# Kernel tuning notes

Measured on AMD Instinct MI355X. Metric: run time of the kernel, lower is better.

## Reference

```python
import jax, jax.numpy as jnp
import numpy as np

N = 100000      # nodes
E = 1600000     # directed edges (avg degree 16)
F_IN = 128
HID = 128
C = 40
EPS = 1e-5      # BatchNorm1d default eps


def setup_inputs() -> dict:
    key = jax.random.key(0)
    ks = jax.random.split(key, 8)
    f32 = jnp.float32
    x = jax.random.normal(ks[0], (N, F_IN), f32)
    edge_index = jax.random.randint(ks[1], (2, E), 0, N, dtype=jnp.int32)
    # Glorot-ish init for GCNConv linear weights
    W1 = jax.random.normal(ks[2], (F_IN, HID), f32) / np.float32(np.sqrt(F_IN))
    W2 = jax.random.normal(ks[3], (HID, HID), f32) / np.float32(np.sqrt(HID))
    W3 = jax.random.normal(ks[4], (HID, C), f32) / np.float32(np.sqrt(HID))
    return {
        "x": x, "edge_index": edge_index,
        "W1": W1, "b1": jnp.zeros((HID,), f32),
        "gamma1": jnp.ones((HID,), f32), "beta1": jnp.zeros((HID,), f32),
        "W2": W2, "b2": jnp.zeros((HID,), f32),
        "gamma2": jnp.ones((HID,), f32), "beta2": jnp.zeros((HID,), f32),
        "W3": W3, "b3": jnp.zeros((C,), f32),
    }


def _gcn_norm(edge_index):
    # PyG GCNConv default: add self loops, symmetric normalization
    loops = jnp.arange(N, dtype=edge_index.dtype)
    row = jnp.concatenate([edge_index[0], loops])  # source
    col = jnp.concatenate([edge_index[1], loops])  # destination
    deg = jax.ops.segment_sum(jnp.ones(row.shape[0], jnp.float32), col, num_segments=N)
    dinv = jnp.where(deg > 0, jax.lax.rsqrt(deg), 0.0)
    norm = dinv[row] * dinv[col]  # [E+N]
    return row, col, norm


def _gcn_conv(h, W, b, row, col, norm):
    h = h @ W                                   # [N, out]
    msg = h[row] * norm[:, None]                # gather + scale per edge
    out = jax.ops.segment_sum(msg, col, num_segments=N)
    return out + b


def _batchnorm(h, gamma, beta):
    # training-mode batch statistics (biased variance), as torch BatchNorm1d
    mean = h.mean(axis=0)
    var = ((h - mean) ** 2).mean(axis=0)
    return gamma * (h - mean) * jax.lax.rsqrt(var + EPS) + beta


def reference(x, edge_index, W1, b1, gamma1, beta1, W2, b2, gamma2, beta2, W3, b3):
    row, col, norm = _gcn_norm(edge_index)
    h = _gcn_conv(x, W1, b1, row, col, norm)
    h = jax.nn.relu(_batchnorm(h, gamma1, beta1))
    h = _gcn_conv(h, W2, b2, row, col, norm)
    h = jax.nn.relu(_batchnorm(h, gamma2, beta2))
    h = _gcn_conv(h, W3, b3, row, col, norm)
    return jax.nn.log_softmax(h, axis=1)
```

## Files before the change

kernel.cpp:

```cpp
#include <hip/hip_runtime.h>
#include <math.h>

#define N_NODES 100000
#define N_EDGES 1600000
#define NCLS 40
#define BN_EPS 1e-5f

#define BSPAN 256
#define NBKT 391
#define GBIN 256
#define CHUNK (N_EDGES / GBIN)
#define ECAP 5120

typedef unsigned int u32;
typedef unsigned short u16;
typedef __attribute__((ext_vector_type(8))) short bf16x8;
typedef __attribute__((ext_vector_type(4))) float f32x4;

__device__ inline float bl_lo(u32 u) { u32 x = u << 16; return __builtin_bit_cast(float, x); }
__device__ inline float bl_hi(u32 u) { u32 x = u & 0xFFFF0000u; return __builtin_bit_cast(float, x); }
__device__ inline u16 f2bl(float f) {
    u32 x = __builtin_bit_cast(u32, f);
    return (u16)((x + 0x7FFFu + ((x >> 16) & 1u)) >> 16);
}
__device__ inline u32 pk2(float lo, float hi) { return (u32)f2bl(lo) | ((u32)f2bl(hi) << 16); }

__global__ __launch_bounds__(256) void binA_kernel(const int* __restrict__ ei,
                                                   u32* __restrict__ ebuf,
                                                   int* __restrict__ runstart) {
    __shared__ int hist[NBKT];
    __shared__ int tmp[256];
    const int s = blockIdx.x, tid = threadIdx.x;
    const int e0 = s * CHUNK;

    for (int b = tid; b < NBKT; b += 256) hist[b] = 0;
    __syncthreads();
    for (int j = tid; j < CHUNK; j += 256) {
        int dst = ei[N_EDGES + e0 + j];
        atomicAdd(&hist[dst >> 8], 1);
    }
    __syncthreads();
    int i0 = 2 * tid, i1 = 2 * tid + 1;
    int a = (i0 < NBKT) ? hist[i0] : 0;
    int c = (i1 < NBKT) ? hist[i1] : 0;
    int ps = a + c;
    tmp[tid] = ps;
    __syncthreads();
    for (int o = 1; o < 256; o <<= 1) {
        int t = (tid >= o) ? tmp[tid - o] : 0;
        __syncthreads();
        tmp[tid] += t;
        __syncthreads();
    }
    int excl = tmp[tid] - ps;
    if (i0 < NBKT) hist[i0] = excl;
    if (i1 < NBKT) hist[i1] = excl + a;
    __syncthreads();
    for (int b = tid; b < NBKT; b += 256) runstart[b * GBIN + s] = hist[b];
    if (tid == 0) runstart[NBKT * GBIN + s] = CHUNK;
    __syncthreads();
    for (int j = tid; j < CHUNK; j += 256) {
        int src = ei[e0 + j];
        int dst = ei[N_EDGES + e0 + j];
        int p = atomicAdd(&hist[dst >> 8], 1);
        ebuf[e0 + p] = (u32)src | ((u32)(dst & 255) << 17);
    }
}

__global__ __launch_bounds__(256) void binC_kernel(const u32* __restrict__ ebuf,
                                                   const int* __restrict__ runstart,
                                                   int* __restrict__ csr, int* __restrict__ offs,
                                                   float* __restrict__ dinv) {
    __shared__ int srcs[ECAP];
    __shared__ unsigned char dl8[ECAP];
    __shared__ int sorted[ECAP + BSPAN];
    __shared__ int nodecnt[BSPAN];
    __shared__ int cursor[BSPAN];
    __shared__ int tmp[256];
    __shared__ int sbase;
    const int b = blockIdx.x, tid = threadIdx.x;
    const int nb0 = b * BSPAN;
    const int nnod = min(BSPAN, N_NODES - nb0);

    int r0 = runstart[b * GBIN + tid];
    int r1 = runstart[(b + 1) * GBIN + tid];
    int len = r1 - r0;

    tmp[tid] = r0;
    __syncthreads();
    for (int o = 128; o >= 1; o >>= 1) {
        if (tid < o) tmp[tid] += tmp[tid + o];
        __syncthreads();
    }
    if (tid == 0) sbase = tmp[0] + nb0;
    __syncthreads();
    const int base = sbase;

    tmp[tid] = len;
    __syncthreads();
    for (int o = 1; o < 256; o <<= 1) {
        int t = (tid >= o) ? tmp[tid - o] : 0;
        __syncthreads();
        tmp[tid] += t;
        __syncthreads();
    }
    int myoff = tmp[tid] - len;
    int total_e = tmp[255];
    if (total_e > ECAP) total_e = ECAP;
    for (int n = tid; n < BSPAN; n += 256) nodecnt[n] = 0;
    __syncthreads();
    const u32* seg = ebuf + (size_t)tid * CHUNK + r0;
    for (int j = 0; j < len; ++j) {
        int idx = myoff + j;
        if (idx >= ECAP) break;
        u32 p = seg[j];
        srcs[idx] = (int)(p & 0x1FFFFu);
        int dl = (int)(p >> 17);
        dl8[idx] = (unsigned char)dl;
        atomicAdd(&nodecnt[dl], 1);
    }
    __syncthreads();
    int cnt = (tid < nnod) ? (nodecnt[tid] + 1) : 0;
    tmp[tid] = cnt;
    __syncthreads();
    for (int o = 1; o < 256; o <<= 1) {
        int t = (tid >= o) ? tmp[tid - o] : 0;
        __syncthreads();
        tmp[tid] += t;
        __syncthreads();
    }
    int noff = tmp[tid] - cnt;
    if (tid < nnod) {
        cursor[tid] = noff + 1;
        sorted[noff] = nb0 + tid;
        offs[nb0 + tid] = base + noff;
        dinv[nb0 + tid] = rsqrtf((float)(nodecnt[tid] + 1));
    }
    if (b == NBKT - 1 && tid == 0) offs[N_NODES] = N_EDGES + N_NODES;
    __syncthreads();
    for (int idx = tid; idx < total_e; idx += 256) {
        int dl = dl8[idx];
        int p = atomicAdd(&cursor[dl], 1);
        sorted[p] = srcs[idx];
    }
    __syncthreads();
    int tot = total_e + nnod;
    for (int idx = tid; idx < tot; idx += 256) csr[base + idx] = sorted[idx];
}

__global__ void prep_w(const float* __restrict__ W1, const float* __restrict__ W2,
                       const float* __restrict__ W3, u16* __restrict__ Wt1,
                       u16* __restrict__ Wt2, u16* __restrict__ Wt3) {
    int b = blockIdx.x, t = threadIdx.x;
    if (b == 0) {
        for (int idx = t; idx < 128 * 128; idx += 256) {
            int c = idx >> 7, k = idx & 127;
            Wt1[idx] = f2bl(W1[k * 128 + c]);
        }
    } else if (b == 1) {
        for (int idx = t; idx < 128 * 128; idx += 256) {
            int c = idx >> 7, k = idx & 127;
            Wt2[idx] = f2bl(W2[k * 128 + c]);
        }
    } else {
        for (int idx = t; idx < 48 * 128; idx += 256) {
            int c = idx >> 7, k = idx & 127;
            Wt3[idx] = (c < NCLS) ? f2bl(W3[k * NCLS + c]) : (u16)0;
        }
    }
}

template <bool FOLD, bool IN_BF16, int BN, int OUTMODE>
__global__ __launch_bounds__(256) void mfma_gemm(const void* __restrict__ Xv,
                                                 const u16* __restrict__ Wt,
                                                 const float* __restrict__ ac,
                                                 const float* __restrict__ dinv,
                                                 void* __restrict__ Yv) {
    __shared__ __align__(16) u16 sX[64 * 128];
    __shared__ __align__(16) u16 sW[BN * 128];
    const int tid = threadIdx.x;
    const int row0 = blockIdx.x * 64;

    for (int ci = tid; ci < BN * 16; ci += 256) {
        int n = ci >> 4, ch = ci & 15;
        uint4 v = *(const uint4*)(Wt + n * 128 + ch * 8);
        *(uint4*)&sW[n * 128 + ((ch ^ (n & 7)) * 8)] = v;
    }
    {
        int r = tid >> 2;
        int gr = row0 + r;
        if (gr >= N_NODES) gr = N_NODES - 1;
        #pragma unroll
        for (int i = 0; i < 4; ++i) {
            int ch = (tid & 3) * 4 + i;
            int k0 = ch * 8;
            float xv[8];
            if (IN_BF16) {
                uint4 v = *((const uint4*)Xv + (size_t)gr * 16 + ch);
                xv[0] = bl_lo(v.x); xv[1] = bl_hi(v.x);
                xv[2] = bl_lo(v.y); xv[3] = bl_hi(v.y);
                xv[4] = bl_lo(v.z); xv[5] = bl_hi(v.z);
                xv[6] = bl_lo(v.w); xv[7] = bl_hi(v.w);
            } else {
                float4 p = *((const float4*)Xv + (size_t)gr * 32 + ch * 2);
                float4 q = *((const float4*)Xv + (size_t)gr * 32 + ch * 2 + 1);
                xv[0] = p.x; xv[1] = p.y; xv[2] = p.z; xv[3] = p.w;
                xv[4] = q.x; xv[5] = q.y; xv[6] = q.z; xv[7] = q.w;
            }
            if (FOLD) {
                #pragma unroll
                for (int j = 0; j < 8; ++j)
                    xv[j] = fmaxf(fmaf(xv[j], ac[k0 + j], ac[128 + k0 + j]), 0.f);
            }
            uint4 w;
            w.x = pk2(xv[0], xv[1]); w.y = pk2(xv[2], xv[3]);
            w.z = pk2(xv[4], xv[5]); w.w = pk2(xv[6], xv[7]);
            *(uint4*)&sX[r * 128 + ((ch ^ (r & 7)) * 8)] = w;
        }
    }
    __syncthreads();

    const int w = tid >> 6, l = tid & 63;
    const int g = l >> 4;
    const int lrow = w * 16 + (l & 15);
    bf16x8 afrag[4];
    #pragma unroll
    for (int kc = 0; kc < 4; ++kc) {
        int ch = kc * 4 + g;
        afrag[kc] = *(const bf16x8*)&sX[lrow * 128 + ((ch ^ (lrow & 7)) * 8)];
    }
    float sc[4];
    #pragma unroll
    for (int r = 0; r < 4; ++r) {
        int row = row0 + w * 16 + g * 4 + r;
        sc[r] = (row < N_NODES) ? dinv[row] : 0.f;
    }
    #pragma unroll
    for (int cg = 0; cg < BN / 16; ++cg) {
        const int n = cg * 16 + (l & 15);
        f32x4 acc = {0.f, 0.f, 0.f, 0.f};
        #pragma unroll
        for (int kc = 0; kc < 4; ++kc) {
            int ch = kc * 4 + g;
            bf16x8 bfrag = *(const bf16x8*)&sW[n * 128 + ((ch ^ (n & 7)) * 8)];
            acc = __builtin_amdgcn_mfma_f32_16x16x32_bf16(afrag[kc], bfrag, acc, 0, 0, 0);
        }
        #pragma unroll
        for (int r = 0; r < 4; ++r) {
            int row = row0 + w * 16 + g * 4 + r;
            if (row < N_NODES) {
                if (OUTMODE == 0) {
                    ((u16*)Yv)[(size_t)row * 128 + n] = f2bl(acc[r] * sc[r]);
                } else {
                    if (n < NCLS) ((u16*)Yv)[(size_t)row * NCLS + n] = f2bl(acc[r] * sc[r]);
                }
            }
        }
    }
}

__global__ __launch_bounds__(64) void agg_kernel(const u32* __restrict__ hin,
                                                 const float* __restrict__ dinv,
                                                 const int* __restrict__ offs,
                                                 const int* __restrict__ csr,
                                                 const float* __restrict__ bias,
                                                 u32* __restrict__ hout) {
    const int i = blockIdx.x;
    const int f = threadIdx.x;
    const float di = dinv[i];
    const int e0 = offs[i], e1 = offs[i + 1];
    float al[8] = {}, ah[8] = {};
    int e = e0;
    for (; e + 8 <= e1; e += 8) {
        int s[8];
        #pragma unroll
        for (int j = 0; j < 8; ++j) s[j] = csr[e + j];
        #pragma unroll
        for (int j = 0; j < 8; ++j) {
            u32 u = hin[(size_t)s[j] * 64 + f];
            al[j] += bl_lo(u);
            ah[j] += bl_hi(u);
        }
    }
    if (e + 4 <= e1) {
        int s[4];
        #pragma unroll
        for (int j = 0; j < 4; ++j) s[j] = csr[e + j];
        #pragma unroll
        for (int j = 0; j < 4; ++j) {
            u32 u = hin[(size_t)s[j] * 64 + f];
            al[j] += bl_lo(u);
            ah[j] += bl_hi(u);
        }
        e += 4;
    }
    for (; e < e1; ++e) {
        u32 u = hin[(size_t)csr[e] * 64 + f];
        al[0] += bl_lo(u);
        ah[0] += bl_hi(u);
    }
    float rl = ((al[0] + al[1]) + (al[2] + al[3])) + ((al[4] + al[5]) + (al[6] + al[7]));
    float rh = ((ah[0] + ah[1]) + (ah[2] + ah[3])) + ((ah[4] + ah[5]) + (ah[6] + ah[7]));
    rl = fmaf(rl, di, bias[2 * f]);
    rh = fmaf(rh, di, bias[2 * f + 1]);
    hout[(size_t)i * 64 + f] = pk2(rl, rh);
}

__global__ __launch_bounds__(256) void stats_kernel(const u32* __restrict__ h,
                                                    float* __restrict__ stats) {
    __shared__ float sm[4 * 256];
    const int tid = threadIdx.x;
    const int lane = tid & 63, wv = tid >> 6;
    const int wid = blockIdx.x * 4 + wv;
    const int nw = gridDim.x * 4;
    float s[8] = {}, q[8] = {};
    for (int quad = wid; quad < N_NODES / 4; quad += nw) {
        uint4 v = *(const uint4*)(h + (size_t)quad * 256 + lane * 4);
        float f;
        f = bl_lo(v.x); s[0] += f; q[0] = fmaf(f, f, q[0]);
        f = bl_hi(v.x); s[1] += f; q[1] = fmaf(f, f, q[1]);
        f = bl_lo(v.y); s[2] += f; q[2] = fmaf(f, f, q[2]);
        f = bl_hi(v.y); s[3] += f; q[3] = fmaf(f, f, q[3]);
        f = bl_lo(v.z); s[4] += f; q[4] = fmaf(f, f, q[4]);
        f = bl_hi(v.z); s[5] += f; q[5] = fmaf(f, f, q[5]);
        f = bl_lo(v.w); s[6] += f; q[6] = fmaf(f, f, q[6]);
        f = bl_hi(v.w); s[7] += f; q[7] = fmaf(f, f, q[7]);
    }
    #pragma unroll
    for (int j = 0; j < 8; ++j) {
        s[j] += __shfl_xor(s[j], 16); s[j] += __shfl_xor(s[j], 32);
        q[j] += __shfl_xor(q[j], 16); q[j] += __shfl_xor(q[j], 32);
    }
    if (lane < 16) {
        #pragma unroll
        for (int j = 0; j < 8; ++j) {
            sm[wv * 256 + 8 * lane + j] = s[j];
            sm[wv * 256 + 128 + 8 * lane + j] = q[j];
        }
    }
    __syncthreads();
    float v = sm[tid] + sm[256 + tid] + sm[512 + tid] + sm[768 + tid];
    atomicAdd(&stats[tid], v);
}

__global__ void finalize_kernel(const float* __restrict__ stats, const float* __restrict__ gamma,
                                const float* __restrict__ beta, float* __restrict__ ac) {
    int f = threadIdx.x;
    float mean = stats[f] * (1.f / N_NODES);
    float var = stats[128 + f] * (1.f / N_NODES) - mean * mean;
    float a = gamma[f] * rsqrtf(var + BN_EPS);
    ac[f] = a;
    ac[128 + f] = fmaf(-mean, a, beta[f]);
}

__global__ __launch_bounds__(64) void agg_lsm_kernel(const u32* __restrict__ hin,
                                                     const float* __restrict__ dinv,
                                                     const int* __restrict__ offs,
                                                     const int* __restrict__ csr,
                                                     const float* __restrict__ bias,
                                                     float* __restrict__ out) {
    const int i = blockIdx.x;
    const int lane = threadIdx.x;
    const int es = lane / 20;
    const int cp = lane - es * 20;
    const bool act = es < 3;
    const float di = dinv[i];
    const int e0 = offs[i], e1 = offs[i + 1];
    float al[4] = {}, ah[4] = {};
    if (act) {
        int ej = e0 + es;
        for (; ej + 9 < e1; ej += 12) {
            int s0 = csr[ej], s1 = csr[ej + 3], s2 = csr[ej + 6], s3 = csr[ej + 9];
            u32 u0 = hin[(size_t)s0 * 20 + cp];
            u32 u1 = hin[(size_t)s1 * 20 + cp];
            u32 u2 = hin[(size_t)s2 * 20 + cp];
            u32 u3 = hin[(size_t)s3 * 20 + cp];
            al[0] += bl_lo(u0); ah[0] += bl_hi(u0);
            al[1] += bl_lo(u1); ah[1] += bl_hi(u1);
            al[2] += bl_lo(u2); ah[2] += bl_hi(u2);
            al[3] += bl_lo(u3); ah[3] += bl_hi(u3);
        }
        for (; ej < e1; ej += 3) {
            u32 u = hin[(size_t)csr[ej] * 20 + cp];
            al[0] += bl_lo(u);
            ah[0] += bl_hi(u);
        }
    }
    float a = (al[0] + al[1]) + (al[2] + al[3]);
    float h = (ah[0] + ah[1]) + (ah[2] + ah[3]);
    float a1 = __shfl(a, cp + 20), a2 = __shfl(a, cp + 40);
    float h1 = __shfl(h, cp + 20), h2 = __shfl(h, cp + 40);
    float lo = fmaf(a + a1 + a2, di, bias[2 * cp]);
    float hi = fmaf(h + h1 + h2, di, bias[2 * cp + 1]);
    float m = (lane < 20) ? fmaxf(lo, hi) : -INFINITY;
    #pragma unroll
    for (int o = 32; o >= 1; o >>= 1) m = fmaxf(m, __shfl_xor(m, o));
    float ex = (lane < 20) ? (__expf(lo - m) + __expf(hi - m)) : 0.f;
    float sum = ex;
    #pragma unroll
    for (int o = 32; o >= 1; o >>= 1) sum += __shfl_xor(sum, o);
    float lse = m + __logf(sum);
    if (lane < 20) {
        float2 r = make_float2(lo - lse, hi - lse);
        *((float2*)out + (size_t)i * 20 + cp) = r;
    }
}

extern "C" void kernel_launch(void* const* d_in, const int* in_sizes, int n_in,
                              void* d_out, int out_size, void* d_ws, size_t ws_size,
                              hipStream_t stream) {
    const float* x   = (const float*)d_in[0];
    const int*   ei  = (const int*)d_in[1];
    const float* W1  = (const float*)d_in[2];
    const float* b1  = (const float*)d_in[3];
    const float* g1  = (const float*)d_in[4];
    const float* be1 = (const float*)d_in[5];
    const float* W2  = (const float*)d_in[6];
    const float* b2  = (const float*)d_in[7];
    const float* g2  = (const float*)d_in[8];
    const float* be2 = (const float*)d_in[9];
    const float* W3  = (const float*)d_in[10];
    const float* b3  = (const float*)d_in[11];
    float* out = (float*)d_out;

    char* w = (char*)d_ws;
    size_t off = 0;
    auto take = [&](size_t bytes) {
        void* p = w + off;
        off = (off + bytes + 255) & ~(size_t)255;
        return p;
    };
    float* dinv   = (float*)take((size_t)N_NODES * 4);
    int*   offs   = (int*)take((size_t)(N_NODES + 1) * 4);
    int*   csr    = (int*)take((size_t)(N_EDGES + N_NODES) * 4);
    float* stats1 = (float*)take(256 * 4);
    float* stats2 = (float*)take(256 * 4);
    float* ac1    = (float*)take(256 * 4);
    float* ac2    = (float*)take(256 * 4);
    u16*   Wt1    = (u16*)take(128 * 128 * 2);
    u16*   Wt2    = (u16*)take(128 * 128 * 2);
    u16*   Wt3    = (u16*)take(48 * 128 * 2);
    u32*   bufA   = (u32*)take((size_t)N_NODES * 64 * 4);
    u32*   bufB   = (u32*)take((size_t)N_NODES * 64 * 4);

    u32*  ebuf     = (u32*)bufA;
    int*  runstart = (int*)bufB;
    u32*  Y3       = (u32*)bufA;

    hipMemsetAsync(stats1, 0, 256 * 4, stream);
    hipMemsetAsync(stats2, 0, 256 * 4, stream);

    prep_w<<<3, 256, 0, stream>>>(W1, W2, W3, Wt1, Wt2, Wt3);
    binA_kernel<<<GBIN, 256, 0, stream>>>(ei, ebuf, runstart);
    binC_kernel<<<NBKT, 256, 0, stream>>>(ebuf, runstart, csr, offs, dinv);

    const int gm = (N_NODES + 63) / 64;
    mfma_gemm<false, false, 128, 0><<<gm, 256, 0, stream>>>(x, Wt1, nullptr, dinv, bufA);
    agg_kernel<<<N_NODES, 64, 0, stream>>>(bufA, dinv, offs, csr, b1, bufB);
    stats_kernel<<<512, 256, 0, stream>>>(bufB, stats1);
    finalize_kernel<<<1, 128, 0, stream>>>(stats1, g1, be1, ac1);
    mfma_gemm<true, true, 128, 0><<<gm, 256, 0, stream>>>(bufB, Wt2, ac1, dinv, bufA);
    agg_kernel<<<N_NODES, 64, 0, stream>>>(bufA, dinv, offs, csr, b2, bufB);
    stats_kernel<<<512, 256, 0, stream>>>(bufB, stats2);
    finalize_kernel<<<1, 128, 0, stream>>>(stats2, g2, be2, ac2);
    mfma_gemm<true, true, 48, 1><<<gm, 256, 0, stream>>>(bufB, Wt3, ac2, dinv, Y3);
    agg_lsm_kernel<<<N_NODES, 64, 0, stream>>>(Y3, dinv, offs, csr, b3, out);
}
```

Before: 353.2 us.

## Vectorize aggregation gathers across edge groups and fold stats zeroing into prep

The aggregation kernels now split each wave into edge groups, with each lane loading 16-byte (or 8-byte for the final layer) chunks of a neighbor row. Several edges are processed in parallel and combined with cross-lane shuffles, instead of every lane loading one 4-byte word per edge. This aims to cut the number of memory instructions and raise memory-level parallelism in the gather-bound aggregation. The two stats memsets are also replaced by an extra block in prep_w to save launch overhead. The cost is extra shuffle reductions, and only a quarter of the lanes do useful work at the output write.

```diff
diff --git a/kernel.cpp b/kernel.cpp
--- a/kernel.cpp
+++ b/kernel.cpp
@@ -150,7 +150,8 @@
 
 __global__ void prep_w(const float* __restrict__ W1, const float* __restrict__ W2,
                        const float* __restrict__ W3, u16* __restrict__ Wt1,
-                       u16* __restrict__ Wt2, u16* __restrict__ Wt3) {
+                       u16* __restrict__ Wt2, u16* __restrict__ Wt3,
+                       float* __restrict__ stats1, float* __restrict__ stats2) {
     int b = blockIdx.x, t = threadIdx.x;
     if (b == 0) {
         for (int idx = t; idx < 128 * 128; idx += 256) {
@@ -162,11 +163,14 @@
             int c = idx >> 7, k = idx & 127;
             Wt2[idx] = f2bl(W2[k * 128 + c]);
         }
-    } else {
+    } else if (b == 2) {
         for (int idx = t; idx < 48 * 128; idx += 256) {
             int c = idx >> 7, k = idx & 127;
             Wt3[idx] = (c < NCLS) ? f2bl(W3[k * NCLS + c]) : (u16)0;
         }
+    } else {
+        stats1[t] = 0.f;
+        stats2[t] = 0.f;
     }
 }
 
@@ -266,44 +270,54 @@
                                                  const float* __restrict__ bias,
                                                  u32* __restrict__ hout) {
     const int i = blockIdx.x;
-    const int f = threadIdx.x;
+    const int l = threadIdx.x;
+    const int g = l >> 4, c = l & 15;
     const float di = dinv[i];
     const int e0 = offs[i], e1 = offs[i + 1];
-    float al[8] = {}, ah[8] = {};
+    float a[8] = {};
     int e = e0;
     for (; e + 8 <= e1; e += 8) {
-        int s[8];
-        #pragma unroll
-        for (int j = 0; j < 8; ++j) s[j] = csr[e + j];
-        #pragma unroll
-        for (int j = 0; j < 8; ++j) {
-            u32 u = hin[(size_t)s[j] * 64 + f];
-            al[j] += bl_lo(u);
-            ah[j] += bl_hi(u);
-        }
+        int sA = csr[e + g];
+        int sB = csr[e + 4 + g];
+        uint4 uA = *(const uint4*)(hin + (size_t)sA * 64 + c * 4);
+        uint4 uB = *(const uint4*)(hin + (size_t)sB * 64 + c * 4);
+        a[0] += bl_lo(uA.x); a[1] += bl_hi(uA.x); a[2] += bl_lo(uA.y); a[3] += bl_hi(uA.y);
+        a[4] += bl_lo(uA.z); a[5] += bl_hi(uA.z); a[6] += bl_lo(uA.w); a[7] += bl_hi(uA.w);
+        a[0] += bl_lo(uB.x); a[1] += bl_hi(uB.x); a[2] += bl_lo(uB.y); a[3] += bl_hi(uB.y);
+        a[4] += bl_lo(uB.z); a[5] += bl_hi(uB.z); a[6] += bl_lo(uB.w); a[7] += bl_hi(uB.w);
     }
     if (e + 4 <= e1) {
-        int s[4];
-        #pragma unroll
-        for (int j = 0; j < 4; ++j) s[j] = csr[e + j];
-        #pragma unroll
-        for (int j = 0; j < 4; ++j) {
-            u32 u = hin[(size_t)s[j] * 64 + f];
-            al[j] += bl_lo(u);
-            ah[j] += bl_hi(u);
-        }
+        int s = csr[e + g];
+        uint4 u = *(const uint4*)(hin + (size_t)s * 64 + c * 4);
+        a[0] += bl_lo(u.x); a[1] += bl_hi(u.x); a[2] += bl_lo(u.y); a[3] += bl_hi(u.y);
+        a[4] += bl_lo(u.z); a[5] += bl_hi(u.z); a[6] += bl_lo(u.w); a[7] += bl_hi(u.w);
         e += 4;
     }
-    for (; e < e1; ++e) {
-        u32 u = hin[(size_t)csr[e] * 64 + f];
-        al[0] += bl_lo(u);
-        ah[0] += bl_hi(u);
-    }
-    float rl = ((al[0] + al[1]) + (al[2] + al[3])) + ((al[4] + al[5]) + (al[6] + al[7]));
-    float rh = ((ah[0] + ah[1]) + (ah[2] + ah[3])) + ((ah[4] + ah[5]) + (ah[6] + ah[7]));
-    rl = fmaf(rl, di, bias[2 * f]);
-    rh = fmaf(rh, di, bias[2 * f + 1]);
-    hout[(size_t)i * 64 + f] = pk2(rl, rh);
+    if (e < e1) {
+        int idx = e + g;
+        bool on = idx < e1;
+        int s = csr[on ? idx : (e1 - 1)];
+        uint4 u = *(const uint4*)(hin + (size_t)s * 64 + c * 4);
+        if (on) {
+            a[0] += bl_lo(u.x); a[1] += bl_hi(u.x); a[2] += bl_lo(u.y); a[3] += bl_hi(u.y);
+            a[4] += bl_lo(u.z); a[5] += bl_hi(u.z); a[6] += bl_lo(u.w); a[7] += bl_hi(u.w);
+        }
+    }
+    #pragma unroll
+    for (int j = 0; j < 8; ++j) {
+        a[j] += __shfl_xor(a[j], 16);
+        a[j] += __shfl_xor(a[j], 32);
+    }
+    if (l < 16) {
+        float4 b0 = *(const float4*)(bias + c * 8);
+        float4 b1 = *(const float4*)(bias + c * 8 + 4);
+        uint4 o;
+        o.x = pk2(fmaf(a[0], di, b0.x), fmaf(a[1], di, b0.y));
+        o.y = pk2(fmaf(a[2], di, b0.z), fmaf(a[3], di, b0.w));
+        o.z = pk2(fmaf(a[4], di, b1.x), fmaf(a[5], di, b1.y));
+        o.w = pk2(fmaf(a[6], di, b1.z), fmaf(a[7], di, b1.w));
+        *(uint4*)(hout + (size_t)i * 64 + c * 4) = o;
+    }
 }
 
 __global__ __launch_bounds__(256) void stats_kernel(const u32* __restrict__ h,
@@ -360,49 +374,67 @@
                                                      const float* __restrict__ bias,
                                                      float* __restrict__ out) {
     const int i = blockIdx.x;
-    const int lane = threadIdx.x;
-    const int es = lane / 20;
-    const int cp = lane - es * 20;
-    const bool act = es < 3;
+    const int l = threadIdx.x;
+    int g = l / 10;
+    const int c = l - g * 10;
+    const bool act = g < 6;
+    if (!act) g = 5;
     const float di = dinv[i];
     const int e0 = offs[i], e1 = offs[i + 1];
-    float al[4] = {}, ah[4] = {};
-    if (act) {
-        int ej = e0 + es;
-        for (; ej + 9 < e1; ej += 12) {
-            int s0 = csr[ej], s1 = csr[ej + 3], s2 = csr[ej + 6], s3 = csr[ej + 9];
-            u32 u0 = hin[(size_t)s0 * 20 + cp];
-            u32 u1 = hin[(size_t)s1 * 20 + cp];
-            u32 u2 = hin[(size_t)s2 * 20 + cp];
-            u32 u3 = hin[(size_t)s3 * 20 + cp];
-            al[0] += bl_lo(u0); ah[0] += bl_hi(u0);
-            al[1] += bl_lo(u1); ah[1] += bl_hi(u1);
-            al[2] += bl_lo(u2); ah[2] += bl_hi(u2);
-            al[3] += bl_lo(u3); ah[3] += bl_hi(u3);
-        }
-        for (; ej < e1; ej += 3) {
-            u32 u = hin[(size_t)csr[ej] * 20 + cp];
-            al[0] += bl_lo(u);
-            ah[0] += bl_hi(u);
-        }
-    }
-    float a = (al[0] + al[1]) + (al[2] + al[3]);
-    float h = (ah[0] + ah[1]) + (ah[2] + ah[3]);
-    float a1 = __shfl(a, cp + 20), a2 = __shfl(a, cp + 40);
-    float h1 = __shfl(h, cp + 20), h2 = __shfl(h, cp + 40);
-    float lo = fmaf(a + a1 + a2, di, bias[2 * cp]);
-    float hi = fmaf(h + h1 + h2, di, bias[2 * cp + 1]);
-    float m = (lane < 20) ? fmaxf(lo, hi) : -INFINITY;
+    float a[4] = {};
+    int e = e0;
+    for (; e + 12 <= e1; e += 12) {
+        int sA = csr[e + g];
+        int sB = csr[e + 6 + g];
+        uint2 uA = *(const uint2*)(hin + (size_t)sA * 20 + c * 2);
+        uint2 uB = *(const uint2*)(hin + (size_t)sB * 20 + c * 2);
+        if (act) {
+            a[0] += bl_lo(uA.x); a[1] += bl_hi(uA.x); a[2] += bl_lo(uA.y); a[3] += bl_hi(uA.y);
+            a[0] += bl_lo(uB.x); a[1] += bl_hi(uB.x); a[2] += bl_lo(uB.y); a[3] += bl_hi(uB.y);
+        }
+    }
+    if (e + 6 <= e1) {
+        int s = csr[e + g];
+        uint2 u = *(const uint2*)(hin + (size_t)s * 20 + c * 2);
+        if (act) {
+            a[0] += bl_lo(u.x); a[1] += bl_hi(u.x); a[2] += bl_lo(u.y); a[3] += bl_hi(u.y);
+        }
+        e += 6;
+    }
+    if (e < e1) {
+        int idx = e + g;
+        bool on = act && (idx < e1);
+        int s = csr[on ? idx : (e1 - 1)];
+        uint2 u = *(const uint2*)(hin + (size_t)s * 20 + c * 2);
+        if (on) {
+            a[0] += bl_lo(u.x); a[1] += bl_hi(u.x); a[2] += bl_lo(u.y); a[3] += bl_hi(u.y);
+        }
+    }
+    #pragma unroll
+    for (int j = 0; j < 4; ++j) {
+        a[j] += __shfl(a[j], (l + 30) & 63);
+        float t1 = __shfl(a[j], (l + 10) & 63);
+        float t2 = __shfl(a[j], (l + 20) & 63);
+        a[j] += t1 + t2;
+    }
+    float v0 = 0.f, v1 = 0.f, v2 = 0.f, v3 = 0.f;
+    if (l < 10) {
+        v0 = fmaf(a[0], di, bias[c * 4 + 0]);
+        v1 = fmaf(a[1], di, bias[c * 4 + 1]);
+        v2 = fmaf(a[2], di, bias[c * 4 + 2]);
+        v3 = fmaf(a[3], di, bias[c * 4 + 3]);
+    }
+    float m = (l < 10) ? fmaxf(fmaxf(v0, v1), fmaxf(v2, v3)) : -INFINITY;
     #pragma unroll
     for (int o = 32; o >= 1; o >>= 1) m = fmaxf(m, __shfl_xor(m, o));
-    float ex = (lane < 20) ? (__expf(lo - m) + __expf(hi - m)) : 0.f;
+    float ex = (l < 10) ? (__expf(v0 - m) + __expf(v1 - m) + __expf(v2 - m) + __expf(v3 - m)) : 0.f;
     float sum = ex;
     #pragma unroll
     for (int o = 32; o >= 1; o >>= 1) sum += __shfl_xor(sum, o);
     float lse = m + __logf(sum);
-    if (lane < 20) {
-        float2 r = make_float2(lo - lse, hi - lse);
-        *((float2*)out + (size_t)i * 20 + cp) = r;
+    if (l < 10) {
+        float4 r = make_float4(v0 - lse, v1 - lse, v2 - lse, v3 - lse);
+        *((float4*)(out + (size_t)i * 40) + c) = r;
     }
 }
 
@@ -447,10 +479,7 @@
     int*  runstart = (int*)bufB;
     u32*  Y3       = (u32*)bufA;
 
-    hipMemsetAsync(stats1, 0, 256 * 4, stream);
-    hipMemsetAsync(stats2, 0, 256 * 4, stream);
-
-    prep_w<<<3, 256, 0, stream>>>(W1, W2, W3, Wt1, Wt2, Wt3);
+    prep_w<<<4, 256, 0, stream>>>(W1, W2, W3, Wt1, Wt2, Wt3, stats1, stats2);
     binA_kernel<<<GBIN, 256, 0, stream>>>(ei, ebuf, runstart);
     binC_kernel<<<NBKT, 256, 0, stream>>>(ebuf, runstart, csr, offs, dinv);
 
```

Result: faster. 345.3 us (-2.2%).
